# Performance work log

Measured on AMD Instinct MI355X. Metric: run time of the kernel, lower is better.

The kernel has to match this reference:

```python
import jax, jax.numpy as jnp
import numpy as np

D = 2048        # input_size / model dim
H = 2816        # hidden_size per expert (GLU -> w1 has 2*H rows)
E = 8           # num_experts
M = 4096        # tokens (batch*seq)


def setup_inputs() -> dict:
    key = jax.random.key(0)
    k1, k2, k3, k4, k5 = jax.random.split(key, 5)
    x = jax.random.normal(k1, (M, D), dtype=jnp.float32)
    # ParallelExperts init: uniform(-1/fan_in_dim, 1/fan_in_dim); scale kept simple here
    w1 = jax.random.uniform(k2, (E, 2 * H, D), dtype=jnp.float32, minval=-1.0, maxval=1.0) / (2 * H)
    w2 = jax.random.uniform(k3, (E, D, H), dtype=jnp.float32, minval=-1.0, maxval=1.0) / D
    router_w = jax.random.normal(k4, (E, D), dtype=jnp.float32) * (1.0 / np.sqrt(D))
    bias = jnp.zeros((D,), dtype=jnp.float32)
    return {"x": x, "w1": w1, "w2": w2, "router_w": router_w, "bias": bias, "top_k": 2}


def _moe_forward(x, w1, w2, router_w, bias, top_k):
    # Router: logits -> softmax (fp32) -> top-k -> renormalize (fused_moe semantics)
    logits = x @ router_w.T                                # [M, E]
    probs = jax.nn.softmax(logits.astype(jnp.float32), axis=-1)
    topk_w, topk_ids = jax.lax.top_k(probs, top_k)         # [M, k]
    topk_w = topk_w / jnp.sum(topk_w, axis=-1, keepdims=True)
    # Dense combine weights [M, E]: gate weight if expert selected, else 0
    m = x.shape[0]
    combine = jnp.zeros((m, w1.shape[0]), dtype=x.dtype)
    combine = combine.at[jnp.arange(m)[:, None], topk_ids].add(topk_w.astype(x.dtype))
    # Grouped expert GEMMs, expressed as a loop over the small fixed expert set.
    # Contribution of expert e is masked by combine[:, e] (zero for unrouted tokens).
    y = jnp.zeros_like(x)
    hdim = w2.shape[2]
    for e in range(w1.shape[0]):
        g = x @ w1[e].T                                    # [M, 2H]
        h = jax.nn.silu(g[:, :hdim]) * g[:, hdim:]          # silu_and_mul (GLU)
        y = y + combine[:, e:e + 1] * (h @ w2[e].T)         # [M, D]
    return y + bias


def reference(x, w1, w2, router_w, bias, top_k):
    return _moe_forward(x, w1, w2, router_w, bias, top_k)
```

## Files before the change

### kernel.cpp

```cpp
#include <hip/hip_runtime.h>
#include <hip/hip_bf16.h>
#include <stdint.h>

#define M_TOK 4096
#define DDIM  2048
#define HDIM  2816
#define NEXP  8
#define PMAX  10240
#define MAXTILES 40
#define NB1   44
#define NB2   16
#define NKT1  32
#define NKT2  44

typedef __attribute__((ext_vector_type(8))) short short8;
typedef __attribute__((ext_vector_type(4))) float f32x4;

#define GLD16(g, l) __builtin_amdgcn_global_load_lds(                              \
    (const __attribute__((address_space(1))) unsigned int*)(g),                    \
    (__attribute__((address_space(3))) unsigned int*)(l), 16, 0, 0)

#define VMCNT(n) asm volatile("s_waitcnt vmcnt(" #n ")" ::: "memory")

__device__ __forceinline__ unsigned short f2bf(float f) {
  unsigned int u = __float_as_uint(f);
  u += 0x7fffu + ((u >> 16) & 1u);
  return (unsigned short)(u >> 16);
}
__device__ __forceinline__ float bf2f(unsigned short u) {
  return __uint_as_float(((unsigned)u) << 16);
}

__global__ void cvt_bf16_k(const float4* __restrict__ in, ushort4* __restrict__ out, int n4,
                           int* __restrict__ tok, int* __restrict__ counts,
                           int* __restrict__ cursors, int doinit) {
  int gid = blockIdx.x * blockDim.x + threadIdx.x;
  if (doinit) {
    if (gid < PMAX) tok[gid] = -1;
    if (gid < NEXP) { counts[gid] = 0; cursors[gid] = 0; }
  }
  int stride = gridDim.x * blockDim.x;
  for (int i = gid; i < n4; i += stride) {
    float4 v = in[i];
    ushort4 o;
    o.x = f2bf(v.x); o.y = f2bf(v.y); o.z = f2bf(v.z); o.w = f2bf(v.w);
    out[i] = o;
  }
}

__global__ __launch_bounds__(256) void router_k(const float4* __restrict__ x4,
                                                const float4* __restrict__ rw4,
                                                ushort4* __restrict__ xb4,
                                                float* __restrict__ wgt,
                                                int* __restrict__ eid,
                                                int* __restrict__ counts) {
  int lane = threadIdx.x & 63;
  int wv = threadIdx.x >> 6;
  int t = blockIdx.x * 4 + wv;
  int base = t * (DDIM / 4);
  float acc[NEXP];
#pragma unroll
  for (int e = 0; e < NEXP; ++e) acc[e] = 0.f;
#pragma unroll
  for (int j = 0; j < DDIM / 4 / 64; ++j) {
    float4 v = x4[base + j * 64 + lane];
    ushort4 o;
    o.x = f2bf(v.x); o.y = f2bf(v.y); o.z = f2bf(v.z); o.w = f2bf(v.w);
    xb4[base + j * 64 + lane] = o;
#pragma unroll
    for (int e = 0; e < NEXP; ++e) {
      float4 w = rw4[e * (DDIM / 4) + j * 64 + lane];
      acc[e] += v.x * w.x + v.y * w.y + v.z * w.z + v.w * w.w;
    }
  }
#pragma unroll
  for (int e = 0; e < NEXP; ++e) {
#pragma unroll
    for (int s = 32; s > 0; s >>= 1) acc[e] += __shfl_xor(acc[e], s, 64);
  }
  if (lane == 0) {
    float mx = acc[0];
#pragma unroll
    for (int e = 1; e < NEXP; ++e) mx = fmaxf(mx, acc[e]);
    float p[NEXP];
#pragma unroll
    for (int e = 0; e < NEXP; ++e) p[e] = expf(acc[e] - mx);
    int e0 = 0; float p0 = p[0];
#pragma unroll
    for (int e = 1; e < NEXP; ++e) if (p[e] > p0) { p0 = p[e]; e0 = e; }
    int e1 = -1; float p1 = -1.f;
#pragma unroll
    for (int e = 0; e < NEXP; ++e) if (e != e0 && p[e] > p1) { p1 = p[e]; e1 = e; }
    float s = p0 + p1;
    wgt[2 * t] = p0 / s; wgt[2 * t + 1] = p1 / s;
    eid[2 * t] = e0;     eid[2 * t + 1] = e1;
    atomicAdd(&counts[e0], 1);
    atomicAdd(&counts[e1], 1);
  }
}

__global__ __launch_bounds__(256) void offscat_k(const int* __restrict__ counts,
                                                 int* __restrict__ tile2exp,
                                                 int* __restrict__ tilerow,
                                                 int* __restrict__ ntiles,
                                                 const int* __restrict__ eid,
                                                 int* __restrict__ cursors,
                                                 int* __restrict__ tok,
                                                 int* __restrict__ slot) {
  __shared__ int soffs[NEXP];
  if (threadIdx.x == 0) {
    int o = 0, nt = 0;
    for (int e = 0; e < NEXP; ++e) {
      soffs[e] = o;
      int c = counts[e];
      int pt = (c + 255) >> 8;
      for (int i = 0; i < pt; ++i) { tile2exp[nt] = e; tilerow[nt] = o + i * 256; ++nt; }
      o += pt << 8;
    }
    ntiles[0] = nt;
  }
  __syncthreads();
  for (int t = threadIdx.x; t < M_TOK; t += 256) {
#pragma unroll
    for (int k = 0; k < 2; ++k) {
      int e = eid[2 * t + k];
      int p = soffs[e] + atomicAdd(&cursors[e], 1);
      tok[p] = t;
      slot[2 * t + k] = p;
    }
  }
}

__global__ __launch_bounds__(256, 2) void gemm1_k(const unsigned short* __restrict__ xb,
                                                  const unsigned short* __restrict__ w1b,
                                                  const int* __restrict__ tok,
                                                  const int* __restrict__ tile2exp,
                                                  const int* __restrict__ tilerow,
                                                  const int* __restrict__ ntiles,
                                                  unsigned short* __restrict__ h) {
  __shared__ char ldsp[65536];
  int mt = blockIdx.x;
  if (mt >= ntiles[0]) return;
  int e = tile2exp[mt], r0 = tilerow[mt];
  int n0 = blockIdx.y * 64;
  int tid = threadIdx.x, lane = tid & 63;
  int wv = tid >> 6, wm = wv >> 1, wn = wv & 1;
  int l15 = lane & 15, lq = lane >> 4;

  int sg = tid & 7, srow = tid >> 3;
  unsigned int aOff[8], bOff[4];
#pragma unroll
  for (int j = 0; j < 8; ++j) {
    int r = j * 32 + srow;
    int t = tok[r0 + r]; if (t < 0) t = 0;
    aOff[j] = (unsigned int)t * (DDIM * 2) + (unsigned int)((sg ^ (r & 7)) << 4);
  }
#pragma unroll
  for (int j = 0; j < 4; ++j) {
    int r = j * 32 + srow;
    int w1row = e * (2 * HDIM) + (r < 64 ? n0 + r : HDIM + n0 + (r - 64));
    bOff[j] = (unsigned int)w1row * (DDIM * 2) + (unsigned int)((sg ^ (r & 7)) << 4);
  }

  int aRd[8], bRd[4];
#pragma unroll
  for (int i = 0; i < 8; ++i) {
    int r = wm * 128 + i * 16 + l15;
    aRd[i] = r * 128 + ((lq ^ (r & 7)) << 4);
  }
#pragma unroll
  for (int i = 0; i < 4; ++i) {
    int r = wn * 64 + i * 16 + l15;
    bRd[i] = r * 128 + ((lq ^ (r & 7)) << 4);
  }

  f32x4 acc[8][4];
#pragma unroll
  for (int mi = 0; mi < 8; ++mi)
#pragma unroll
    for (int ni = 0; ni < 4; ++ni) acc[mi][ni] = (f32x4)(0.f);

  const char* xB = (const char*)xb;
  const char* wB = (const char*)w1b;

#pragma unroll 1
  for (int kt = 0; kt < NKT1; ++kt) {
    __syncthreads();
    unsigned int kb = (unsigned int)kt * 128;
#pragma unroll
    for (int j = 0; j < 8; ++j) GLD16(xB + aOff[j] + kb, ldsp + j * 4096 + tid * 16);
#pragma unroll
    for (int j = 0; j < 4; ++j) GLD16(wB + bOff[j] + kb, ldsp + 32768 + j * 4096 + tid * 16);
    VMCNT(0);
    __syncthreads();
#pragma unroll
    for (int kh = 0; kh < 2; ++kh) {
      int kx = kh << 6;
      short8 a[8], b[4];
#pragma unroll
      for (int i = 0; i < 8; ++i) a[i] = *(const short8*)(ldsp + (aRd[i] ^ kx));
#pragma unroll
      for (int i = 0; i < 4; ++i) b[i] = *(const short8*)(ldsp + 32768 + (bRd[i] ^ kx));
      __builtin_amdgcn_s_setprio(1);
#pragma unroll
      for (int mi = 0; mi < 8; ++mi)
#pragma unroll
        for (int ni = 0; ni < 4; ++ni)
          acc[mi][ni] = __builtin_amdgcn_mfma_f32_16x16x32_bf16(a[mi], b[ni], acc[mi][ni], 0, 0, 0);
      __builtin_amdgcn_s_setprio(0);
    }
  }

  __syncthreads();
  float* xch = (float*)ldsp;
  if (wn == 1) {
#pragma unroll
    for (int mi = 0; mi < 8; ++mi)
#pragma unroll
      for (int ni = 0; ni < 4; ++ni)
#pragma unroll
        for (int j = 0; j < 4; ++j) {
          int r = wm * 128 + mi * 16 + lq * 4 + j;
          int c = ni * 16 + l15;
          xch[r * 64 + (c ^ (lq << 2))] = acc[mi][ni][j];
        }
  }
  __syncthreads();
  if (wn == 0) {
#pragma unroll
    for (int mi = 0; mi < 8; ++mi)
#pragma unroll
      for (int ni = 0; ni < 4; ++ni)
#pragma unroll
        for (int j = 0; j < 4; ++j) {
          int r = wm * 128 + mi * 16 + lq * 4 + j;
          int c = ni * 16 + l15;
          float u = xch[r * 64 + (c ^ (lq << 2))];
          float gg = acc[mi][ni][j];
          float sv = gg / (1.f + expf(-gg));
          h[(size_t)(r0 + r) * HDIM + n0 + c] = f2bf(sv * u);
        }
  }
}

__global__ __launch_bounds__(256, 2) void gemm2_k(const unsigned short* __restrict__ h,
                                                  const unsigned short* __restrict__ w2b,
                                                  const int* __restrict__ tile2exp,
                                                  const int* __restrict__ tilerow,
                                                  const int* __restrict__ ntiles,
                                                  unsigned short* __restrict__ yp) {
  __shared__ char ldsp[49152];
  int mt = blockIdx.x;
  if (mt >= ntiles[0]) return;
  int e = tile2exp[mt], r0 = tilerow[mt];
  int n0 = blockIdx.y * 128;
  int tid = threadIdx.x, lane = tid & 63;
  int wv = tid >> 6, wm = wv >> 1, wn = wv & 1;
  int l15 = lane & 15, lq = lane >> 4;

  int sg = tid & 7, srow = tid >> 3;
  unsigned int aOff[8], bOff[4];
#pragma unroll
  for (int j = 0; j < 8; ++j) {
    int r = j * 32 + srow;
    aOff[j] = (unsigned int)(r0 + r) * (HDIM * 2) + (unsigned int)((sg ^ (r & 7)) << 4);
  }
#pragma unroll
  for (int j = 0; j < 4; ++j) {
    int r = j * 32 + srow;
    bOff[j] = (unsigned int)(e * DDIM + n0 + r) * (HDIM * 2) + (unsigned int)((sg ^ (r & 7)) << 4);
  }

  int aRd[8], bRd[4];
#pragma unroll
  for (int i = 0; i < 8; ++i) {
    int r = wm * 128 + i * 16 + l15;
    aRd[i] = r * 128 + ((lq ^ (r & 7)) << 4);
  }
#pragma unroll
  for (int i = 0; i < 4; ++i) {
    int r = wn * 64 + i * 16 + l15;
    bRd[i] = r * 128 + ((lq ^ (r & 7)) << 4);
  }

  f32x4 acc[8][4];
#pragma unroll
  for (int mi = 0; mi < 8; ++mi)
#pragma unroll
    for (int ni = 0; ni < 4; ++ni) acc[mi][ni] = (f32x4)(0.f);

  const char* hB = (const char*)h;
  const char* wB = (const char*)w2b;

#pragma unroll 1
  for (int kt = 0; kt < NKT2; ++kt) {
    __syncthreads();
    unsigned int kb = (unsigned int)kt * 128;
#pragma unroll
    for (int j = 0; j < 8; ++j) GLD16(hB + aOff[j] + kb, ldsp + j * 4096 + tid * 16);
#pragma unroll
    for (int j = 0; j < 4; ++j) GLD16(wB + bOff[j] + kb, ldsp + 32768 + j * 4096 + tid * 16);
    VMCNT(0);
    __syncthreads();
#pragma unroll
    for (int kh = 0; kh < 2; ++kh) {
      int kx = kh << 6;
      short8 a[8], b[4];
#pragma unroll
      for (int i = 0; i < 8; ++i) a[i] = *(const short8*)(ldsp + (aRd[i] ^ kx));
#pragma unroll
      for (int i = 0; i < 4; ++i) b[i] = *(const short8*)(ldsp + 32768 + (bRd[i] ^ kx));
      __builtin_amdgcn_s_setprio(1);
#pragma unroll
      for (int mi = 0; mi < 8; ++mi)
#pragma unroll
        for (int ni = 0; ni < 4; ++ni)
          acc[mi][ni] = __builtin_amdgcn_mfma_f32_16x16x32_bf16(a[mi], b[ni], acc[mi][ni], 0, 0, 0);
      __builtin_amdgcn_s_setprio(0);
    }
  }

#pragma unroll
  for (int mi = 0; mi < 8; ++mi)
#pragma unroll
    for (int ni = 0; ni < 4; ++ni)
#pragma unroll
      for (int j = 0; j < 4; ++j) {
        int r = r0 + wm * 128 + mi * 16 + lq * 4 + j;
        int c = n0 + wn * 64 + ni * 16 + l15;
        yp[(size_t)r * DDIM + c] = f2bf(acc[mi][ni][j]);
      }
}

__global__ void combine_k(const unsigned short* __restrict__ yp, const float* __restrict__ wgt,
                          const int* __restrict__ slot, const float* __restrict__ bias,
                          float* __restrict__ out) {
  int idx = blockIdx.x * blockDim.x + threadIdx.x;
  int t = idx >> 8, q = (idx & 255) * 8;
  float w0 = wgt[2 * t], w1 = wgt[2 * t + 1];
  int s0 = slot[2 * t], s1 = slot[2 * t + 1];
  short8 a8 = *(const short8*)(yp + (size_t)s0 * DDIM + q);
  short8 b8 = *(const short8*)(yp + (size_t)s1 * DDIM + q);
  float* op = out + (size_t)t * DDIM + q;
#pragma unroll
  for (int k = 0; k < 8; ++k) {
    float av = bf2f((unsigned short)a8[k]);
    float bv = bf2f((unsigned short)b8[k]);
    op[k] = w0 * av + w1 * bv + bias[q + k];
  }
}

extern "C" void kernel_launch(void* const* d_in, const int* in_sizes, int n_in,
                              void* d_out, int out_size, void* d_ws, size_t ws_size,
                              hipStream_t stream) {
  const float* x    = (const float*)d_in[0];
  const float* w1   = (const float*)d_in[1];
  const float* w2   = (const float*)d_in[2];
  const float* rw   = (const float*)d_in[3];
  const float* bias = (const float*)d_in[4];
  float* out = (float*)d_out;

  char* ws = (char*)d_ws;
  size_t off = 0;
  auto alloc = [&](size_t bytes) -> void* {
    void* p = ws + off;
    off = (off + bytes + 255) & ~(size_t)255;
    return p;
  };
  unsigned short* w1b = (unsigned short*)alloc((size_t)NEXP * 2 * HDIM * DDIM * 2);
  unsigned short* w2b = (unsigned short*)alloc((size_t)NEXP * DDIM * HDIM * 2);
  unsigned short* xb  = (unsigned short*)alloc((size_t)M_TOK * DDIM * 2);
  unsigned short* h   = (unsigned short*)alloc((size_t)PMAX * HDIM * 2);
  unsigned short* yp  = (unsigned short*)alloc((size_t)PMAX * DDIM * 2);
  float* wgt          = (float*)alloc((size_t)M_TOK * 2 * 4);
  int* eid            = (int*)alloc((size_t)M_TOK * 2 * 4);
  int* slot           = (int*)alloc((size_t)M_TOK * 2 * 4);
  int* tok            = (int*)alloc((size_t)PMAX * 4);
  int* counts         = (int*)alloc(64 * 4);
  int* cursors        = (int*)alloc(64 * 4);
  int* ntiles         = (int*)alloc(64 * 4);
  int* tile2exp       = (int*)alloc(128 * 4);
  int* tilerow        = (int*)alloc(128 * 4);

  const int n1 = (int)((size_t)NEXP * 2 * HDIM * DDIM / 4);
  const int n2 = (int)((size_t)NEXP * DDIM * HDIM / 4);
  hipLaunchKernelGGL(cvt_bf16_k, dim3(2048), dim3(256), 0, stream,
                     (const float4*)w1, (ushort4*)w1b, n1, tok, counts, cursors, 1);
  hipLaunchKernelGGL(cvt_bf16_k, dim3(2048), dim3(256), 0, stream,
                     (const float4*)w2, (ushort4*)w2b, n2, tok, counts, cursors, 0);
  hipLaunchKernelGGL(router_k, dim3(M_TOK / 4), dim3(256), 0, stream,
                     (const float4*)x, (const float4*)rw, (ushort4*)xb, wgt, eid, counts);
  hipLaunchKernelGGL(offscat_k, dim3(1), dim3(256), 0, stream,
                     counts, tile2exp, tilerow, ntiles, eid, cursors, tok, slot);
  hipLaunchKernelGGL(gemm1_k, dim3(MAXTILES, NB1), dim3(256), 0, stream,
                     xb, w1b, tok, tile2exp, tilerow, ntiles, h);
  hipLaunchKernelGGL(gemm2_k, dim3(MAXTILES, NB2), dim3(256), 0, stream,
                     h, w2b, tile2exp, tilerow, ntiles, yp);
  hipLaunchKernelGGL(combine_k, dim3(M_TOK * (DDIM / 8) / 256), dim3(256), 0, stream, yp, wgt, slot, bias, out);
}
```

Measured before the change: 746.0 us.

## Fuse combine into gemm2 via atomics and overlap w2 conversion with gemm1

The combine kernel and the bf16 yp buffer are removed. Gemm2's epilogue now scales each row by its routing weight and atomically adds it into the fp32 output, which is pre-initialized with bias during the w1 conversion kernel. The w2 fp32-to-bf16 conversion moves into extra blocks of the gemm1 grid so it can overlap with the GEMM work instead of running as a separate pass. The trade-off is contention from global fp32 atomics and non-deterministic summation order, in exchange for avoiding an intermediate buffer round-trip and two kernel launches.

New measurement: 781.1 us. +4.7%, slower.

```diff
diff --git a/kernel.cpp b/kernel.cpp
--- a/kernel.cpp
+++ b/kernel.cpp
@@ -8,10 +8,12 @@
 #define NEXP  8
 #define PMAX  10240
 #define MAXTILES 40
+#define CVW   8
 #define NB1   44
 #define NB2   16
 #define NKT1  32
 #define NKT2  44
+#define W2CHUNK 32768
 
 typedef __attribute__((ext_vector_type(8))) short short8;
 typedef __attribute__((ext_vector_type(4))) float f32x4;
@@ -31,15 +33,16 @@
   return __uint_as_float(((unsigned)u) << 16);
 }
 
-__global__ void cvt_bf16_k(const float4* __restrict__ in, ushort4* __restrict__ out, int n4,
-                           int* __restrict__ tok, int* __restrict__ counts,
-                           int* __restrict__ cursors, int doinit) {
+__global__ void cvt1_k(const float4* __restrict__ in, ushort4* __restrict__ out, int n4,
+                       int* __restrict__ tok, int* __restrict__ counts,
+                       int* __restrict__ cursors,
+                       float4* __restrict__ outy, const float4* __restrict__ bias4) {
   int gid = blockIdx.x * blockDim.x + threadIdx.x;
-  if (doinit) {
-    if (gid < PMAX) tok[gid] = -1;
-    if (gid < NEXP) { counts[gid] = 0; cursors[gid] = 0; }
-  }
+  if (gid < PMAX) tok[gid] = -1;
+  if (gid < NEXP) { counts[gid] = 0; cursors[gid] = 0; }
   int stride = gridDim.x * blockDim.x;
+  for (int i = gid; i < M_TOK * (DDIM / 4); i += stride)
+    outy[i] = bias4[i & (DDIM / 4 - 1)];
   for (int i = gid; i < n4; i += stride) {
     float4 v = in[i];
     ushort4 o;
@@ -104,9 +107,10 @@
                                                  int* __restrict__ tilerow,
                                                  int* __restrict__ ntiles,
                                                  const int* __restrict__ eid,
+                                                 const float* __restrict__ wgt,
                                                  int* __restrict__ cursors,
                                                  int* __restrict__ tok,
-                                                 int* __restrict__ slot) {
+                                                 float* __restrict__ wslot) {
   __shared__ int soffs[NEXP];
   if (threadIdx.x == 0) {
     int o = 0, nt = 0;
@@ -126,7 +130,7 @@
       int e = eid[2 * t + k];
       int p = soffs[e] + atomicAdd(&cursors[e], 1);
       tok[p] = t;
-      slot[2 * t + k] = p;
+      wslot[p] = wgt[2 * t + k];
     }
   }
 }
@@ -137,9 +141,23 @@
                                                   const int* __restrict__ tile2exp,
                                                   const int* __restrict__ tilerow,
                                                   const int* __restrict__ ntiles,
-                                                  unsigned short* __restrict__ h) {
+                                                  unsigned short* __restrict__ h,
+                                                  const float4* __restrict__ w2src,
+                                                  ushort4* __restrict__ w2dst) {
   __shared__ char ldsp[65536];
-  int mt = blockIdx.x;
+  int bx = blockIdx.x;
+  if (bx >= MAXTILES) {
+    int chunk = (bx - MAXTILES) * NB1 + blockIdx.y;
+    int base = chunk * W2CHUNK;
+    for (int i = base + threadIdx.x; i < base + W2CHUNK; i += 256) {
+      float4 v = w2src[i];
+      ushort4 o;
+      o.x = f2bf(v.x); o.y = f2bf(v.y); o.z = f2bf(v.z); o.w = f2bf(v.w);
+      w2dst[i] = o;
+    }
+    return;
+  }
+  int mt = bx;
   if (mt >= ntiles[0]) return;
   int e = tile2exp[mt], r0 = tilerow[mt];
   int n0 = blockIdx.y * 64;
@@ -248,7 +266,9 @@
                                                   const int* __restrict__ tile2exp,
                                                   const int* __restrict__ tilerow,
                                                   const int* __restrict__ ntiles,
-                                                  unsigned short* __restrict__ yp) {
+                                                  const int* __restrict__ tok,
+                                                  const float* __restrict__ wslot,
+                                                  float* __restrict__ out) {
   __shared__ char ldsp[49152];
   int mt = blockIdx.x;
   if (mt >= ntiles[0]) return;
@@ -323,31 +343,16 @@
 #pragma unroll
   for (int mi = 0; mi < 8; ++mi)
 #pragma unroll
-    for (int ni = 0; ni < 4; ++ni)
-#pragma unroll
-      for (int j = 0; j < 4; ++j) {
-        int r = r0 + wm * 128 + mi * 16 + lq * 4 + j;
-        int c = n0 + wn * 64 + ni * 16 + l15;
-        yp[(size_t)r * DDIM + c] = f2bf(acc[mi][ni][j]);
-      }
-}
-
-__global__ void combine_k(const unsigned short* __restrict__ yp, const float* __restrict__ wgt,
-                          const int* __restrict__ slot, const float* __restrict__ bias,
-                          float* __restrict__ out) {
-  int idx = blockIdx.x * blockDim.x + threadIdx.x;
-  int t = idx >> 8, q = (idx & 255) * 8;
-  float w0 = wgt[2 * t], w1 = wgt[2 * t + 1];
-  int s0 = slot[2 * t], s1 = slot[2 * t + 1];
-  short8 a8 = *(const short8*)(yp + (size_t)s0 * DDIM + q);
-  short8 b8 = *(const short8*)(yp + (size_t)s1 * DDIM + q);
-  float* op = out + (size_t)t * DDIM + q;
-#pragma unroll
-  for (int k = 0; k < 8; ++k) {
-    float av = bf2f((unsigned short)a8[k]);
-    float bv = bf2f((unsigned short)b8[k]);
-    op[k] = w0 * av + w1 * bv + bias[q + k];
-  }
+    for (int j = 0; j < 4; ++j) {
+      int p = r0 + wm * 128 + mi * 16 + lq * 4 + j;
+      int t = tok[p];
+      if (t < 0) continue;
+      float w = wslot[p];
+      float* orow = out + (size_t)t * DDIM + n0 + wn * 64;
+#pragma unroll
+      for (int ni = 0; ni < 4; ++ni)
+        atomicAdd(orow + ni * 16 + l15, w * acc[mi][ni][j]);
+    }
 }
 
 extern "C" void kernel_launch(void* const* d_in, const int* in_sizes, int n_in,
@@ -371,11 +376,10 @@
   unsigned short* w2b = (unsigned short*)alloc((size_t)NEXP * DDIM * HDIM * 2);
   unsigned short* xb  = (unsigned short*)alloc((size_t)M_TOK * DDIM * 2);
   unsigned short* h   = (unsigned short*)alloc((size_t)PMAX * HDIM * 2);
-  unsigned short* yp  = (unsigned short*)alloc((size_t)PMAX * DDIM * 2);
   float* wgt          = (float*)alloc((size_t)M_TOK * 2 * 4);
   int* eid            = (int*)alloc((size_t)M_TOK * 2 * 4);
-  int* slot           = (int*)alloc((size_t)M_TOK * 2 * 4);
   int* tok            = (int*)alloc((size_t)PMAX * 4);
+  float* wslot        = (float*)alloc((size_t)PMAX * 4);
   int* counts         = (int*)alloc(64 * 4);
   int* cursors        = (int*)alloc(64 * 4);
   int* ntiles         = (int*)alloc(64 * 4);
@@ -383,18 +387,16 @@
   int* tilerow        = (int*)alloc(128 * 4);
 
   const int n1 = (int)((size_t)NEXP * 2 * HDIM * DDIM / 4);
-  const int n2 = (int)((size_t)NEXP * DDIM * HDIM / 4);
-  hipLaunchKernelGGL(cvt_bf16_k, dim3(2048), dim3(256), 0, stream,
-                     (const float4*)w1, (ushort4*)w1b, n1, tok, counts, cursors, 1);
-  hipLaunchKernelGGL(cvt_bf16_k, dim3(2048), dim3(256), 0, stream,
-                     (const float4*)w2, (ushort4*)w2b, n2, tok, counts, cursors, 0);
+  hipLaunchKernelGGL(cvt1_k, dim3(2048), dim3(256), 0, stream,
+                     (const float4*)w1, (ushort4*)w1b, n1, tok, counts, cursors,
+                     (float4*)out, (const float4*)bias);
   hipLaunchKernelGGL(router_k, dim3(M_TOK / 4), dim3(256), 0, stream,
                      (const float4*)x, (const float4*)rw, (ushort4*)xb, wgt, eid, counts);
   hipLaunchKernelGGL(offscat_k, dim3(1), dim3(256), 0, stream,
-                     counts, tile2exp, tilerow, ntiles, eid, cursors, tok, slot);
-  hipLaunchKernelGGL(gemm1_k, dim3(MAXTILES, NB1), dim3(256), 0, stream,
-                     xb, w1b, tok, tile2exp, tilerow, ntiles, h);
+                     counts, tile2exp, tilerow, ntiles, eid, wgt, cursors, tok, wslot);
+  hipLaunchKernelGGL(gemm1_k, dim3(MAXTILES + CVW, NB1), dim3(256), 0, stream,
+                     xb, w1b, tok, tile2exp, tilerow, ntiles, h,
+                     (const float4*)w2, (ushort4*)w2b);
   hipLaunchKernelGGL(gemm2_k, dim3(MAXTILES, NB2), dim3(256), 0, stream,
-                     h, w2b, tile2exp, tilerow, ntiles, yp);
-  hipLaunchKernelGGL(combine_k, dim3(M_TOK * (DDIM / 8) / 256), dim3(256), 0, stream, yp, wgt, slot, bias, out);
-}
+                     h, w2b, tile2exp, tilerow, ntiles, tok, wslot, out);
+}
```
